# Performance work log

Hardware: AMD Instinct MI355X
Metric: run time of the kernel (lower is better)

## Reference

```python
import jax, jax.numpy as jnp
import numpy as np

D_MODEL = 1024
NUM_HEADS = 16
HEAD_DIM = D_MODEL // NUM_HEADS


def setup_inputs() -> dict:
    key = jax.random.key(0)
    ks = jax.random.split(key, 12)
    B, S, D = 4, 2048, D_MODEL
    s = 1.0 / np.sqrt(D)
    return {
        "query": jax.random.normal(ks[0], (B, S, D), jnp.float32),
        "key": jax.random.normal(ks[1], (B, S, D), jnp.float32),
        "value": jax.random.normal(ks[2], (B, S, D), jnp.float32),
        "Wq": jax.random.normal(ks[3], (D, D), jnp.float32) * s,
        "bq": jax.random.normal(ks[4], (D,), jnp.float32) * 0.02,
        "Wk": jax.random.normal(ks[5], (D, D), jnp.float32) * s,
        "bk": jax.random.normal(ks[6], (D,), jnp.float32) * 0.02,
        "Wv": jax.random.normal(ks[7], (D, D), jnp.float32) * s,
        "bv": jax.random.normal(ks[8], (D,), jnp.float32) * 0.02,
        "Wo": jax.random.normal(ks[9], (D, D), jnp.float32) * s,
        "bo": jax.random.normal(ks[10], (D,), jnp.float32) * 0.02,
    }


def _split_heads(x):
    B, S, D = x.shape
    return x.reshape(B, S, NUM_HEADS, HEAD_DIM).transpose(0, 2, 1, 3)  # [B,H,S,hd]


def reference(query, key, value, Wq, bq, Wk, bk, Wv, bv, Wo, bo):
    q = _split_heads(query @ Wq + bq)
    k = _split_heads(key @ Wk + bk)
    v = _split_heads(value @ Wv + bv)
    # NOTE: original scales by 1/sqrt(d_model), not 1/sqrt(head_dim)
    scale = 1.0 / np.sqrt(D_MODEL).astype(np.float32)
    scores = jnp.einsum('bhqd,bhkd->bhqk', q, k) * scale  # [B,H,S,S]
    attn = jax.nn.softmax(scores, axis=-1)
    out = jnp.einsum('bhqk,bhkd->bhqd', attn, v)  # [B,H,S,hd]
    B, H, S, hd = out.shape
    out = out.transpose(0, 2, 1, 3).reshape(B, S, D_MODEL)
    out = out @ Wo + bo
    return out, attn
```

## Files before the change

kernel.cpp:

```cpp
#include <hip/hip_runtime.h>
#include <hip/hip_bf16.h>

typedef __bf16 bf16;
typedef __bf16 bf16x8 __attribute__((ext_vector_type(8)));
typedef __bf16 bf16x4 __attribute__((ext_vector_type(4)));
typedef float  f32x4  __attribute__((ext_vector_type(4)));

#define MFMA(A, B, C) __builtin_amdgcn_mfma_f32_16x16x32_bf16((A), (B), (C), 0, 0, 0)

static constexpr int BATCH = 4, S = 2048, D = 1024, NH = 16, HD = 64;
static constexpr int M = BATCH * S;
static constexpr float KL = 0.045084220027780106f;

__device__ __forceinline__ void gload16(const void* g, void* l) {
  __builtin_amdgcn_global_load_lds(
      (const __attribute__((address_space(1))) void*)g,
      (__attribute__((address_space(3))) void*)l, 16, 0, 0);
}

__device__ __forceinline__ float fexp2(float x) {
#if __has_builtin(__builtin_amdgcn_exp2f)
  return __builtin_amdgcn_exp2f(x);
#else
  return exp2f(x);
#endif
}

__global__ __launch_bounds__(256) void wt_convert(
    const float* __restrict__ W0, const float* __restrict__ W1,
    const float* __restrict__ W2, const float* __restrict__ W3,
    bf16* __restrict__ WtAll)
{
  const float* W = blockIdx.y == 0 ? W0 : blockIdx.y == 1 ? W1
                 : blockIdx.y == 2 ? W2 : W3;
  bf16* dst = WtAll + (size_t)blockIdx.y * (D * D);
  int k0 = (blockIdx.x >> 4) * 64, n0 = (blockIdx.x & 15) * 64;
  __shared__ __align__(16) bf16 T[64][72];
  int tid = threadIdx.x;
#pragma unroll
  for (int i = 0; i < 4; ++i) {
    int c = tid + i * 256, r = c >> 4, seg = c & 15;
    float4 v = *reinterpret_cast<const float4*>(W + (size_t)(k0 + r) * D + n0 + seg * 4);
    T[seg * 4 + 0][r] = (bf16)v.x; T[seg * 4 + 1][r] = (bf16)v.y;
    T[seg * 4 + 2][r] = (bf16)v.z; T[seg * 4 + 3][r] = (bf16)v.w;
  }
  __syncthreads();
#pragma unroll
  for (int i = 0; i < 2; ++i) {
    int c = tid + i * 256, r = c >> 3, seg = c & 7;
    *reinterpret_cast<bf16x8*>(dst + (size_t)(n0 + r) * D + k0 + seg * 8) =
        *reinterpret_cast<const bf16x8*>(&T[r][seg * 8]);
  }
}

__global__ __launch_bounds__(256) void x_convert(
    const float* __restrict__ X0, const float* __restrict__ X1,
    const float* __restrict__ X2, bf16* __restrict__ Y)
{
  int t = blockIdx.y;
  const float* X = t == 0 ? X0 : t == 1 ? X1 : X2;
  bf16* Yp = Y + (size_t)t * M * D;
  int idx = blockIdx.x * 256 + threadIdx.x;
#pragma unroll
  for (int i = 0; i < 4; ++i) {
    size_t j = (size_t)idx + (size_t)i * 524288;
    float4 v = reinterpret_cast<const float4*>(X)[j];
    bf16x4 o; o[0] = (bf16)v.x; o[1] = (bf16)v.y; o[2] = (bf16)v.z; o[3] = (bf16)v.w;
    reinterpret_cast<bf16x4*>(Yp)[j] = o;
  }
}

__global__ __launch_bounds__(256) void qkv_gemm(
    const bf16* __restrict__ Xb, const bf16* __restrict__ WtAll,
    const float* __restrict__ bq, const float* __restrict__ bk, const float* __restrict__ bv,
    bf16* __restrict__ Qb, bf16* __restrict__ Kb, bf16* __restrict__ Vtb)
{
  int v = blockIdx.y;
  const bf16*  X    = Xb + (size_t)v * M * D;
  const bf16*  Wt   = WtAll + (size_t)v * (D * D);
  const float* bias = v == 0 ? bq : v == 1 ? bk : bv;

  int x = blockIdx.x;
  int swz = (x & 7) * 64 + (x >> 3);
  int mt = swz >> 3, nt = swz & 7;
  int m0 = mt * 128, n0 = nt * 128;
  int tid = threadIdx.x, lane = tid & 63, w = tid >> 6;
  int wm = (w >> 1) * 64, wn = (w & 1) * 64;
  int lr = lane & 15, lg = lane >> 4;

  __shared__ __align__(16) unsigned char smem[34816];
  auto As = reinterpret_cast<bf16(*)[128][32]>(smem);
  auto Bs = reinterpret_cast<bf16(*)[128][32]>(smem + 16384);

  f32x4 acc[4][4] = {};

  int srow = w * 32 + (lane >> 2);
  int scol = (lane & 3) * 8;

  auto stage = [&](int buf, int ks) {
    const bf16* ga = X + (size_t)(m0 + srow) * D + ks * 32 + scol;
    bf16* la = &As[buf][w * 32][0];
    gload16(ga, la);
    gload16(ga + 16 * D, la + 16 * 32);
    const bf16* gb = Wt + (size_t)(n0 + srow) * D + ks * 32 + scol;
    bf16* lb = &Bs[buf][w * 32][0];
    gload16(gb, lb);
    gload16(gb + 16 * D, lb + 16 * 32);
  };

  stage(0, 0);
  for (int ks = 0; ks < 32; ++ks) {
    __syncthreads();
    if (ks < 31) stage((ks + 1) & 1, ks + 1);
    int buf = ks & 1;
    bf16x8 af[4], bfr[4];
#pragma unroll
    for (int i = 0; i < 4; ++i)
      af[i] = *reinterpret_cast<const bf16x8*>(&As[buf][wm + i * 16 + lr][8 * lg]);
#pragma unroll
    for (int j = 0; j < 4; ++j)
      bfr[j] = *reinterpret_cast<const bf16x8*>(&Bs[buf][wn + j * 16 + lr][8 * lg]);
#pragma unroll
    for (int i = 0; i < 4; ++i)
#pragma unroll
      for (int j = 0; j < 4; ++j)
        acc[i][j] = MFMA(af[i], bfr[j], acc[i][j]);
  }
  __syncthreads();

  if (v < 2) {
    bf16* Out = v == 0 ? Qb : Kb;
    float qs = v == 0 ? KL : 1.0f;
    auto Es = reinterpret_cast<bf16(*)[128]>(smem);
#pragma unroll
    for (int i = 0; i < 4; ++i)
#pragma unroll
      for (int j = 0; j < 4; ++j) {
        int n = wn + j * 16 + lr;
        float bias_n = bias[n0 + n];
#pragma unroll
        for (int r = 0; r < 4; ++r)
          Es[wm + i * 16 + 4 * lg + r][n] = (bf16)((acc[i][j][r] + bias_n) * qs);
      }
    __syncthreads();
#pragma unroll
    for (int i = 0; i < 8; ++i) {
      int c = tid + i * 256, r = c >> 4, seg = c & 15;
      int mg = m0 + r, b = mg >> 11, s = mg & 2047;
      int ng = n0 + seg * 8, h = ng >> 6, d = ng & 63;
      *reinterpret_cast<bf16x8*>(Out + (((size_t)(b * NH + h)) * S + s) * HD + d) =
          *reinterpret_cast<const bf16x8*>(&Es[r][seg * 8]);
    }
  } else {
    auto Es = reinterpret_cast<bf16(*)[136]>(smem);
#pragma unroll
    for (int i = 0; i < 4; ++i)
#pragma unroll
      for (int j = 0; j < 4; ++j) {
        int n = wn + j * 16 + lr;
        float bias_n = bias[n0 + n];
        bf16x4 t;
#pragma unroll
        for (int r = 0; r < 4; ++r) t[r] = (bf16)(acc[i][j][r] + bias_n);
        *reinterpret_cast<bf16x4*>(&Es[n][wm + i * 16 + 4 * lg]) = t;
      }
    __syncthreads();
#pragma unroll
    for (int i = 0; i < 8; ++i) {
      int c = tid + i * 256, r = c >> 4, seg = c & 15;
      int ng = n0 + r, h = ng >> 6, d = ng & 63;
      int mg = m0 + seg * 8, b = mg >> 11, s = mg & 2047;
      *reinterpret_cast<bf16x8*>(Vtb + (((size_t)(b * NH + h)) * HD + d) * S + s) =
          *reinterpret_cast<const bf16x8*>(&Es[r][seg * 8]);
    }
  }
}

__global__ __launch_bounds__(256) void attn_kernel(
    const bf16* __restrict__ Qb, const bf16* __restrict__ Kb, const bf16* __restrict__ Vtb,
    float* __restrict__ attn_out, bf16* __restrict__ ctx)
{
  int xx = blockIdx.x;
  int xcd = xx & 7, r8 = xx >> 3;
  int bh = xcd + 8 * (r8 >> 5);
  int qb = r8 & 31;
  int tid = threadIdx.x, lane = tid & 63, w = tid >> 6;
  int lr = lane & 15, lg = lane >> 4;
  int sw = lr & 7;

  __shared__ __align__(16) bf16 Ks[2][64][64];
  __shared__ __align__(16) bf16 Vs[2][64][64];
  __shared__ __align__(16) bf16 Ps[4][16][40];

  int q_row = qb * 64 + w * 16 + lr;
  const bf16x8* Qp = reinterpret_cast<const bf16x8*>(Qb + ((size_t)bh * S + q_row) * HD);
  bf16x8 qf0 = Qp[lg], qf1 = Qp[4 + lg];

  auto stageK = [&](int buf, int kc) {
    const bf16* base = Kb + ((size_t)bh * S + kc * 64) * HD;
#pragma unroll
    for (int i = 0; i < 2; ++i) {
      int c = i * 256 + tid, row = c >> 3, j = c & 7;
      gload16(base + row * HD + 8 * (j ^ (row & 7)),
              reinterpret_cast<bf16*>(&Ks[buf][0][0]) + c * 8);
    }
  };
  auto stageV = [&](int buf, int kc) {
    const bf16* base = Vtb + (size_t)bh * HD * S + kc * 64;
#pragma unroll
    for (int i = 0; i < 2; ++i) {
      int c = i * 256 + tid, row = c >> 3, j = c & 7;
      gload16(base + (size_t)row * S + 8 * (j ^ (row & 7)),
              reinterpret_cast<bf16*>(&Vs[buf][0][0]) + c * 8);
    }
  };

  float lrun = 0.f;
  stageK(0, 0);
  for (int kc = 0; kc < 32; ++kc) {
    __syncthreads();
    if (kc < 31) stageK((kc + 1) & 1, kc + 1);
    int buf = kc & 1;
#pragma unroll
    for (int sub = 0; sub < 4; ++sub) {
      int row = sub * 16 + lr;
      bf16x8 k0 = *reinterpret_cast<const bf16x8*>(&Ks[buf][row][8 * (lg ^ sw)]);
      bf16x8 k1 = *reinterpret_cast<const bf16x8*>(&Ks[buf][row][8 * ((lg + 4) ^ sw)]);
      f32x4 sa = {};
      sa = MFMA(k0, qf0, sa);
      sa = MFMA(k1, qf1, sa);
      lrun += fexp2(sa[0]) + fexp2(sa[1]) + fexp2(sa[2]) + fexp2(sa[3]);
    }
  }
  lrun += __shfl_xor(lrun, 16);
  lrun += __shfl_xor(lrun, 32);
  float lg2l = __log2f(lrun);

  f32x4 oacc[4] = {};
  float* arow = attn_out + ((size_t)bh * S + q_row) * S;
  stageK(0, 0); stageV(0, 0);
  for (int kc = 0; kc < 32; ++kc) {
    __syncthreads();
    if (kc < 31) { stageK((kc + 1) & 1, kc + 1); stageV((kc + 1) & 1, kc + 1); }
    int buf = kc & 1;
#pragma unroll
    for (int half = 0; half < 2; ++half) {
      f32x4 sg[2];
#pragma unroll
      for (int t = 0; t < 2; ++t) {
        int row = (half * 2 + t) * 16 + lr;
        bf16x8 k0 = *reinterpret_cast<const bf16x8*>(&Ks[buf][row][8 * (lg ^ sw)]);
        bf16x8 k1 = *reinterpret_cast<const bf16x8*>(&Ks[buf][row][8 * ((lg + 4) ^ sw)]);
        f32x4 sa = {};
        sa = MFMA(k0, qf0, sa);
        sa = MFMA(k1, qf1, sa);
        sg[t] = sa;
      }
#pragma unroll
      for (int t = 0; t < 2; ++t) {
        f32x4 pv;
        bf16x4 pb;
#pragma unroll
        for (int r = 0; r < 4; ++r) {
          float p = fexp2(sg[t][r] - lg2l);
          pv[r] = p; pb[r] = (bf16)p;
        }
        __builtin_nontemporal_store(pv,
            reinterpret_cast<f32x4*>(arow + kc * 64 + half * 32 + t * 16 + 4 * lg));
        *reinterpret_cast<bf16x4*>(&Ps[w][lr][t * 16 + 4 * lg]) = pb;
      }
      bf16x8 pa = *reinterpret_cast<const bf16x8*>(&Ps[w][lr][8 * lg]);
#pragma unroll
      for (int dt = 0; dt < 4; ++dt) {
        int vrow = dt * 16 + lr;
        bf16x8 vb = *reinterpret_cast<const bf16x8*>(&Vs[buf][vrow][8 * ((half * 4 + lg) ^ sw)]);
        oacc[dt] = MFMA(pa, vb, oacc[dt]);
      }
    }
  }

  int b = bh >> 4, h = bh & 15;
#pragma unroll
  for (int dt = 0; dt < 4; ++dt)
#pragma unroll
    for (int r = 0; r < 4; ++r) {
      int qr = qb * 64 + w * 16 + 4 * lg + r;
      ctx[((size_t)b * S + qr) * D + h * HD + dt * 16 + lr] = (bf16)oacc[dt][r];
    }
}

__global__ __launch_bounds__(256) void out_gemm(
    const bf16* __restrict__ ctx, const bf16* __restrict__ Wto,
    const float* __restrict__ bo, float* __restrict__ Out)
{
  int x = blockIdx.x;
  int swz = (x & 7) * 64 + (x >> 3);
  int mt = swz >> 3, nt = swz & 7;
  int m0 = mt * 128, n0 = nt * 128;
  int tid = threadIdx.x, lane = tid & 63, w = tid >> 6;
  int wm = (w >> 1) * 64, wn = (w & 1) * 64;
  int lr = lane & 15, lg = lane >> 4;

  __shared__ __align__(16) bf16 As[2][128][32];
  __shared__ __align__(16) bf16 Bs[2][128][32];

  f32x4 acc[4][4] = {};

  int srow = w * 32 + (lane >> 2);
  int scol = (lane & 3) * 8;

  auto stage = [&](int buf, int ks) {
    const bf16* ga = ctx + (size_t)(m0 + srow) * D + ks * 32 + scol;
    bf16* la = &As[buf][w * 32][0];
    gload16(ga, la);
    gload16(ga + 16 * D, la + 16 * 32);
    const bf16* gb = Wto + (size_t)(n0 + srow) * D + ks * 32 + scol;
    bf16* lb = &Bs[buf][w * 32][0];
    gload16(gb, lb);
    gload16(gb + 16 * D, lb + 16 * 32);
  };

  stage(0, 0);
  for (int ks = 0; ks < 32; ++ks) {
    __syncthreads();
    if (ks < 31) stage((ks + 1) & 1, ks + 1);
    int buf = ks & 1;
    bf16x8 af[4], bfr[4];
#pragma unroll
    for (int i = 0; i < 4; ++i)
      af[i] = *reinterpret_cast<const bf16x8*>(&As[buf][wm + i * 16 + lr][8 * lg]);
#pragma unroll
    for (int j = 0; j < 4; ++j)
      bfr[j] = *reinterpret_cast<const bf16x8*>(&Bs[buf][wn + j * 16 + lr][8 * lg]);
#pragma unroll
    for (int i = 0; i < 4; ++i)
#pragma unroll
      for (int j = 0; j < 4; ++j)
        acc[i][j] = MFMA(af[i], bfr[j], acc[i][j]);
  }

#pragma unroll
  for (int i = 0; i < 4; ++i)
#pragma unroll
    for (int j = 0; j < 4; ++j) {
      int n = n0 + wn + j * 16 + lr;
      float bias_n = bo[n];
#pragma unroll
      for (int r = 0; r < 4; ++r)
        Out[(size_t)(m0 + wm + i * 16 + 4 * lg + r) * D + n] = acc[i][j][r] + bias_n;
    }
}

extern "C" void kernel_launch(void* const* d_in, const int* in_sizes, int n_in,
                              void* d_out, int out_size, void* d_ws, size_t ws_size,
                              hipStream_t stream)
{
  const float* query = (const float*)d_in[0];
  const float* key   = (const float*)d_in[1];
  const float* value = (const float*)d_in[2];
  const float* Wq = (const float*)d_in[3]; const float* bq = (const float*)d_in[4];
  const float* Wk = (const float*)d_in[5]; const float* bk = (const float*)d_in[6];
  const float* Wv = (const float*)d_in[7]; const float* bv = (const float*)d_in[8];
  const float* Wo = (const float*)d_in[9]; const float* bo = (const float*)d_in[10];

  float* out  = (float*)d_out;
  float* attn = out + (size_t)M * D;

  char* ws = (char*)d_ws;
  const size_t MiB = 1048576;
  bf16* WtAll = (bf16*)ws;
  bf16* Xb    = (bf16*)(ws + 8 * MiB);
  bf16* Qb    = (bf16*)(ws + 56 * MiB);
  bf16* Kb    = (bf16*)(ws + 72 * MiB);
  bf16* Vtb   = (bf16*)(ws + 88 * MiB);
  bf16* ctx   = Xb;

  wt_convert<<<dim3(256, 4), 256, 0, stream>>>(Wq, Wk, Wv, Wo, WtAll);
  x_convert<<<dim3(2048, 3), 256, 0, stream>>>(query, key, value, Xb);
  qkv_gemm<<<dim3(512, 3), 256, 0, stream>>>(Xb, WtAll, bq, bk, bv, Qb, Kb, Vtb);
  attn_kernel<<<dim3(2048), 256, 0, stream>>>(Qb, Kb, Vtb, attn, ctx);
  out_gemm<<<dim3(512), 256, 0, stream>>>(ctx, WtAll + (size_t)3 * D * D, bo, out);
}
```

Before: 462.1 us.

## Deepen K/V prefetch with explicit vmcnt waits and stage ctx stores through LDS

Swaps __syncthreads in both attention passes for explicit s_waitcnt vmcnt plus raw s_barrier. This lets the next chunk's global-to-LDS loads stay in flight while the current chunk is computed, and the second pass now preloads two chunks. The context epilogue is staged through LDS so each lane writes 16-byte vectors instead of scattered 2-byte bf16 stores. This relies on hand-counted vmcnt values and a reused Ks buffer, which is fragile if the load counts or barriers are wrong.

New measurement: 456.1 us. About the same (-1.3%).

```diff
diff --git a/kernel.cpp b/kernel.cpp
--- a/kernel.cpp
+++ b/kernel.cpp
@@ -25,6 +25,11 @@
   return exp2f(x);
 #endif
 }
+
+#define WAITV_BAR(n)                                        \
+  asm volatile("s_waitcnt vmcnt(" #n ")" ::: "memory");     \
+  __builtin_amdgcn_s_barrier();                             \
+  __builtin_amdgcn_sched_barrier(0);
 
 __global__ __launch_bounds__(256) void wt_convert(
     const float* __restrict__ W0, const float* __restrict__ W1,
@@ -218,8 +223,12 @@
   float lrun = 0.f;
   stageK(0, 0);
   for (int kc = 0; kc < 32; ++kc) {
-    __syncthreads();
-    if (kc < 31) stageK((kc + 1) & 1, kc + 1);
+    if (kc < 31) {
+      stageK((kc + 1) & 1, kc + 1);
+      WAITV_BAR(2)
+    } else {
+      WAITV_BAR(0)
+    }
     int buf = kc & 1;
 #pragma unroll
     for (int sub = 0; sub < 4; ++sub) {
@@ -231,6 +240,7 @@
       sa = MFMA(k1, qf1, sa);
       lrun += fexp2(sa[0]) + fexp2(sa[1]) + fexp2(sa[2]) + fexp2(sa[3]);
     }
+    __builtin_amdgcn_s_barrier();
   }
   lrun += __shfl_xor(lrun, 16);
   lrun += __shfl_xor(lrun, 32);
@@ -238,11 +248,8 @@
 
   f32x4 oacc[4] = {};
   float* arow = attn_out + ((size_t)bh * S + q_row) * S;
-  stageK(0, 0); stageV(0, 0);
-  for (int kc = 0; kc < 32; ++kc) {
-    __syncthreads();
-    if (kc < 31) { stageK((kc + 1) & 1, kc + 1); stageV((kc + 1) & 1, kc + 1); }
-    int buf = kc & 1;
+
+  auto computeB = [&](int buf, int kc) {
 #pragma unroll
     for (int half = 0; half < 2; ++half) {
       f32x4 sg[2];
@@ -277,16 +284,42 @@
         oacc[dt] = MFMA(pa, vb, oacc[dt]);
       }
     }
+  };
+
+  stageK(0, 0); stageV(0, 0);
+  stageK(1, 1); stageV(1, 1);
+  WAITV_BAR(4)
+  computeB(0, 0);
+  __builtin_amdgcn_s_barrier();
+
+  for (int kc = 1; kc < 32; ++kc) {
+    if (kc < 31) {
+      stageK((kc + 1) & 1, kc + 1);
+      stageV((kc + 1) & 1, kc + 1);
+      WAITV_BAR(8)
+    } else {
+      WAITV_BAR(4)
+    }
+    computeB(kc & 1, kc);
+    __builtin_amdgcn_s_barrier();
   }
 
   int b = bh >> 4, h = bh & 15;
+  bf16* cs = reinterpret_cast<bf16*>(&Ks[0][0][0]) + w * (16 * 72);
 #pragma unroll
   for (int dt = 0; dt < 4; ++dt)
 #pragma unroll
-    for (int r = 0; r < 4; ++r) {
-      int qr = qb * 64 + w * 16 + 4 * lg + r;
-      ctx[((size_t)b * S + qr) * D + h * HD + dt * 16 + lr] = (bf16)oacc[dt][r];
-    }
+    for (int r = 0; r < 4; ++r)
+      cs[(4 * lg + r) * 72 + dt * 16 + lr] = (bf16)oacc[dt][r];
+  asm volatile("s_waitcnt lgkmcnt(0)" ::: "memory");
+  __builtin_amdgcn_sched_barrier(0);
+  {
+    int r_ = lane >> 2, cb = (lane & 3) * 16;
+    int qr = qb * 64 + w * 16 + r_;
+    bf16* cp = ctx + ((size_t)b * S + qr) * D + h * HD + cb;
+    *reinterpret_cast<bf16x8*>(cp)     = *reinterpret_cast<const bf16x8*>(&cs[r_ * 72 + cb]);
+    *reinterpret_cast<bf16x8*>(cp + 8) = *reinterpret_cast<const bf16x8*>(&cs[r_ * 72 + cb + 8]);
+  }
 }
 
 __global__ __launch_bounds__(256) void out_gemm(
```
